# Kernel optimization log

Measured on AMD Instinct MI355X. Metric: run time of the kernel, lower is better.

## Reference

```python
import jax, jax.numpy as jnp
import numpy as np
from jax import lax

B, CIN, COUT, H, W, DG, K = 4, 128, 64, 128, 128, 16, 9
MAX_RES = 10.0  # max_residue_magnitude


def conv3x3(x, w, b):
    y = lax.conv_general_dilated(x, w, (1, 1), [(1, 1), (1, 1)],
                                 dimension_numbers=('NCHW', 'OIHW', 'NCHW'))
    return y + b[None, :, None, None]


def setup_inputs() -> dict:
    key = jax.random.key(0)
    ks = jax.random.split(key, 8)
    def rn(k, shape, s=0.05):
        return jax.random.normal(k, shape, jnp.float32) * s
    return {
        "x": jax.random.normal(ks[0], (B, CIN, H, W), jnp.float32),
        "extra_feat": jax.random.normal(ks[1], (B, 3 * COUT, H, W), jnp.float32),
        "w1": rn(ks[2], (COUT, 3 * COUT, 3, 3)), "b1": jnp.zeros((COUT,), jnp.float32),
        "w2": rn(ks[3], (COUT, COUT, 3, 3)), "b2": jnp.zeros((COUT,), jnp.float32),
        "w3": rn(ks[4], (COUT, COUT, 3, 3)), "b3": jnp.zeros((COUT,), jnp.float32),
        "w4": rn(ks[5], (27 * DG, COUT, 3, 3), 0.02), "b4": jnp.zeros((27 * DG,), jnp.float32),
        "weight": rn(ks[6], (COUT, CIN, 3, 3)), "bias": jnp.zeros((COUT,), jnp.float32),
    }


def deform_conv2d(x, offset, mask, weight, bias):
    # Modulated deformable conv, torchvision layout:
    # offset: [B, 2*DG*K, H, W] ordered (group, kernel_pos, (dy,dx))
    # mask:   [B, DG*K, H, W]
    Bn, Cin, Hh, Ww = x.shape
    Cg = Cin // DG
    off = offset.reshape(Bn, DG, K, 2, Hh, Ww)
    dy, dx = off[:, :, :, 0], off[:, :, :, 1]
    m = mask.reshape(Bn, DG, K, Hh, Ww)
    ki = (jnp.arange(K) // 3).reshape(1, 1, K, 1, 1).astype(x.dtype)
    kj = (jnp.arange(K) % 3).reshape(1, 1, K, 1, 1).astype(x.dtype)
    hh = jnp.arange(Hh, dtype=x.dtype).reshape(1, 1, 1, Hh, 1)
    ww = jnp.arange(Ww, dtype=x.dtype).reshape(1, 1, 1, 1, Ww)
    # sampling positions (stride=1, padding=1, dilation=1)
    py = hh - 1.0 + ki + dy  # [B,DG,K,H,W]
    px = ww - 1.0 + kj + dx
    y0 = jnp.floor(py)
    x0 = jnp.floor(px)
    ly = py - y0
    lx = px - x0
    xf = x.reshape(Bn, DG, Cg, Hh * Ww)

    def gather(yi, xi, wgt):
        valid = (yi >= 0) & (yi < Hh) & (xi >= 0) & (xi < Ww)
        yc = jnp.clip(yi, 0, Hh - 1).astype(jnp.int32)
        xc = jnp.clip(xi, 0, Ww - 1).astype(jnp.int32)
        idx = (yc * Ww + xc).reshape(Bn, DG, 1, K * Hh * Ww)
        g = jnp.take_along_axis(xf, jnp.broadcast_to(idx, (Bn, DG, Cg, K * Hh * Ww)), axis=3)
        g = g.reshape(Bn, DG, Cg, K, Hh, Ww)
        w_ = (wgt * valid.astype(x.dtype))[:, :, None]  # [B,DG,1,K,H,W]
        return g * w_

    val = (gather(y0, x0, (1 - ly) * (1 - lx))
           + gather(y0, x0 + 1, (1 - ly) * lx)
           + gather(y0 + 1, x0, ly * (1 - lx))
           + gather(y0 + 1, x0 + 1, ly * lx))
    val = val * m[:, :, None]  # modulation
    wk = weight.reshape(weight.shape[0], DG, Cg, K)
    out = jnp.einsum('bgckhw,ogck->bohw', val, wk) + bias[None, :, None, None]
    return out


def reference(x, extra_feat, w1, b1, w2, b2, w3, b3, w4, b4, weight, bias):
    lrelu = lambda t: jax.nn.leaky_relu(t, 0.1)
    t = lrelu(conv3x3(extra_feat, w1, b1))
    t = lrelu(conv3x3(t, w2, b2))
    t = lrelu(conv3x3(t, w3, b3))
    out = conv3x3(t, w4, b4)
    o1, o2, m = jnp.split(out, 3, axis=1)
    offset = MAX_RES * jnp.tanh(jnp.concatenate([o1, o2], axis=1))
    mask = jax.nn.sigmoid(m)
    return deform_conv2d(x, offset, mask, weight, bias)
```

## Files before the change

### kernel.cpp

```cpp
#include <hip/hip_runtime.h>
#include <cstdint>

#define H_ 128
#define W_ 128
#define HW 16384

typedef _Float16 f16x8 __attribute__((ext_vector_type(8)));
typedef _Float16 f16x4 __attribute__((ext_vector_type(4)));
typedef _Float16 f16x2 __attribute__((ext_vector_type(2)));
typedef float f32x4 __attribute__((ext_vector_type(4)));

__global__ __launch_bounds__(256)
void prep_all(const float* __restrict__ wd, const float* __restrict__ w1,
              const float* __restrict__ w2, const float* __restrict__ w3,
              const float* __restrict__ w4, const float* __restrict__ x,
              const float* __restrict__ ef,
              _Float16* __restrict__ wp, _Float16* __restrict__ A1,
              _Float16* __restrict__ A2, _Float16* __restrict__ A3,
              _Float16* __restrict__ A4, _Float16* __restrict__ xt,
              _Float16* __restrict__ ef_t) {
    __shared__ __align__(16) _Float16 t[128 * 200];
    const int bx  = blockIdx.x;
    const int tid = threadIdx.x;
    if (bx < 384) {
        int i = bx * 256 + tid;
        int kc = i % 96;
        int go = i / 96;
        int o = go & 63, g = go >> 6;
        float v = 0.f;
        if (kc < 72) { int k = kc >> 3, c = kc & 7; v = wd[(o * 128 + g * 8 + c) * 9 + k]; }
        wp[i] = (_Float16)v;
    } else if (bx < 2256) {
        const float* w; _Float16* Ap; int CIN, COUT, COpad, base;
        if (bx < 816)       { w = w1; Ap = A1; CIN = 192; COUT = 64;  COpad = 64;  base = 384; }
        else if (bx < 960)  { w = w2; Ap = A2; CIN = 64;  COUT = 64;  COpad = 64;  base = 816; }
        else if (bx < 1104) { w = w3; Ap = A3; CIN = 64;  COUT = 64;  COpad = 64;  base = 960; }
        else                { w = w4; Ap = A4; CIN = 64;  COUT = 432; COpad = 512; base = 1104; }
        int i = (bx - base) * 256 + tid;
        int kb = i / (COpad * 8);
        int rem = i - kb * (COpad * 8);
        int co = rem >> 3, j = rem & 7;
        int k = kb * 8 + j;
        int s = k / CIN;
        int ci = k - s * CIN;
        int kh = s / 3, kw = s % 3;
        float v = (co < COUT) ? w[((size_t)co * CIN + ci) * 9 + kh * 3 + kw] : 0.f;
        Ap[i] = (_Float16)v;
    } else if (bx < 6352) {
        int i = (bx - 2256) * 256 + tid;
        int px = i & 16383;
        int g  = (i >> 14) & 15;
        int b  = i >> 18;
        const float* xp = x + ((size_t)(b * 128 + g * 8) * HW) + px;
        f16x8 v;
        #pragma unroll
        for (int c = 0; c < 8; ++c) v[c] = (_Float16)xp[c * HW];
        *(f16x8*)(xt + (size_t)i * 8) = v;
    } else {
        int bb = bx - 6352;
        int b = bb >> 7, h = bb & 127;
        for (int i = tid; i < 192 * 128; i += 256) {
            int c = i >> 7, w = i & 127;
            t[w * 200 + c] = (_Float16)ef[((size_t)(b * 192 + c) * 128 + h) * 128 + w];
        }
        __syncthreads();
        _Float16* ob = ef_t + ((size_t)(b * 128 + h) * 128) * 192;
        for (int i = tid; i < 128 * 24; i += 256) {
            int px = i / 24, c8 = i % 24;
            *(f16x8*)(ob + px * 192 + c8 * 8) = *(const f16x8*)(t + px * 200 + c8 * 8);
        }
    }
}

template<int CIN_T, int COpad_T, int NWM, int NWN, int MT, int NT, int ACT>
__global__ __launch_bounds__(256)
void conv_mfma(const _Float16* __restrict__ in, const _Float16* __restrict__ Ap,
               const float* __restrict__ bias, void* __restrict__ outp,
               _Float16* __restrict__ mskp) {
    static_assert(NWM * NWN == 4 && NWN * NT * 16 == 128, "tiling");
    constexpr int NKH = (CIN_T == 64) ? 3 : 1;
    constexpr int NST = 3 / NKH;
    constexpr int CPC = CIN_T / 8;
    constexpr int TC  = NKH * 130 * CPC;
    __shared__ __align__(16) _Float16 lds[TC * 8];

    const int tid  = threadIdx.x;
    const int b    = blockIdx.x >> 7;
    const int h    = blockIdx.x & 127;
    const int cogB = blockIdx.y * (NWM * MT * 16);
    const int wv   = tid >> 6;
    const int wv_m = wv / NWN;
    const int wv_n = wv % NWN;
    const int lane = tid & 63;
    const int quad = lane >> 4;
    const int l16  = lane & 15;

    f32x4 acc[MT][NT];
    #pragma unroll
    for (int mt = 0; mt < MT; ++mt)
        #pragma unroll
        for (int nt = 0; nt < NT; ++nt) acc[mt][nt] = (f32x4){0.f, 0.f, 0.f, 0.f};

    const _Float16* inb = in + (size_t)b * (HW * CIN_T);

    #pragma unroll 1
    for (int s = 0; s < NST; ++s) {
        __syncthreads();
        for (int i = tid; i < TC; i += 256) {
            int kh_l = i / (130 * CPC);
            int r2   = i - kh_l * (130 * CPC);
            int wp_  = r2 / CPC;
            int c8   = r2 - wp_ * CPC;
            int kh   = s * NKH + kh_l;
            int hh   = h - 1 + kh;
            int w    = wp_ - 1;
            f16x8 v = (f16x8){0, 0, 0, 0, 0, 0, 0, 0};
            if ((unsigned)hh < 128u && (unsigned)w < 128u)
                v = *(const f16x8*)(inb + (hh * 128 + w) * CIN_T + c8 * 8);
            int slot = (c8 & ~7) | ((c8 & 7) ^ (wp_ & 7));
            ((f16x8*)lds)[(kh_l * 130 + wp_) * CPC + slot] = v;
        }
        __syncthreads();
        #pragma unroll
        for (int kh_l = 0; kh_l < NKH; ++kh_l) {
            const int kh = s * NKH + kh_l;
            #pragma unroll
            for (int kwi = 0; kwi < 3; ++kwi) {
                #pragma unroll
                for (int ci32 = 0; ci32 < CIN_T / 32; ++ci32) {
                    const int kb0 = (kh * 3 + kwi) * CPC + ci32 * 4;
                    f16x8 aF[MT];
                    #pragma unroll
                    for (int mt = 0; mt < MT; ++mt) {
                        int co_m = cogB + (wv_m * MT + mt) * 16 + l16;
                        aF[mt] = *(const f16x8*)(Ap + ((size_t)(kb0 + quad) * COpad_T + co_m) * 8);
                    }
                    const int c8v = ci32 * 4 + quad;
                    #pragma unroll
                    for (int nt = 0; nt < NT; ++nt) {
                        int n  = (wv_n * NT + nt) * 16 + l16;
                        int wq = n + kwi;
                        int slot = (c8v & ~7) | ((c8v & 7) ^ (wq & 7));
                        f16x8 bF = ((const f16x8*)lds)[(kh_l * 130 + wq) * CPC + slot];
                        #pragma unroll
                        for (int mt = 0; mt < MT; ++mt)
                            acc[mt][nt] = __builtin_amdgcn_mfma_f32_16x16x32_f16(aF[mt], bF, acc[mt][nt], 0, 0, 0);
                    }
                }
            }
        }
    }

    if (ACT == 1) {
        _Float16* ob = (_Float16*)outp + ((size_t)(b * 128 + h) * 128) * 64;
        #pragma unroll
        for (int mt = 0; mt < MT; ++mt) {
            int co_b = (wv_m * MT + mt) * 16 + quad * 4;
            #pragma unroll
            for (int nt = 0; nt < NT; ++nt) {
                int px = (wv_n * NT + nt) * 16 + l16;
                f16x4 sv;
                #pragma unroll
                for (int r = 0; r < 4; ++r) {
                    float v = acc[mt][nt][r] + bias[co_b + r];
                    v = v > 0.f ? v : 0.1f * v;
                    sv[r] = (_Float16)v;
                }
                *(f16x4*)(ob + px * 64 + co_b) = sv;
            }
        }
    } else {
        _Float16* off2 = (_Float16*)outp;
        #pragma unroll
        for (int mt = 0; mt < MT; ++mt) {
            int co_base = cogB + (wv_m * MT + mt) * 16 + quad * 4;
            #pragma unroll
            for (int r2 = 0; r2 < 2; ++r2) {
                int co0 = co_base + 2 * r2;
                if (co0 < 288) {
                    int g = co0 / 18;
                    int k = (co0 - g * 18) >> 1;
                    float bv0 = bias[co0], bv1 = bias[co0 + 1];
                    #pragma unroll
                    for (int nt = 0; nt < NT; ++nt) {
                        int px = (wv_n * NT + nt) * 16 + l16;
                        float v0 = acc[mt][nt][2 * r2]     + bv0;
                        float v1 = acc[mt][nt][2 * r2 + 1] + bv1;
                        float e0 = __expf(2.f * v0);
                        float e1 = __expf(2.f * v1);
                        f16x2 ov;
                        ov[0] = (_Float16)(10.f * (1.f - 2.f / (e0 + 1.f)));
                        ov[1] = (_Float16)(10.f * (1.f - 2.f / (e1 + 1.f)));
                        *(f16x2*)(off2 + (((size_t)(b * 16 + g) * 9 + k) * HW + h * 128 + px) * 2) = ov;
                    }
                } else if (co0 < 432) {
                    #pragma unroll
                    for (int j = 0; j < 2; ++j) {
                        int co = co0 + j;
                        int mm = co - 288;
                        int g = mm / 9;
                        int k = mm - g * 9;
                        float bv = bias[co];
                        #pragma unroll
                        for (int nt = 0; nt < NT; ++nt) {
                            int px = (wv_n * NT + nt) * 16 + l16;
                            float v = acc[mt][nt][2 * r2 + j] + bv;
                            v = 1.f / (1.f + __expf(-v));
                            mskp[((size_t)(b * 16 + g) * 9 + k) * HW + h * 128 + px] = (_Float16)v;
                        }
                    }
                }
            }
        }
    }
}

__global__ __launch_bounds__(256, 4)
void deform_fused(const _Float16* __restrict__ xt, const _Float16* __restrict__ off2,
                  const _Float16* __restrict__ msk, const _Float16* __restrict__ wp,
                  const float* __restrict__ bias, float* __restrict__ out) {
    __shared__ __align__(16) char vlds[2 * 64 * 256];
    const int tid  = threadIdx.x;
    const int bx   = (blockIdx.x & 7) * 128 + (blockIdx.x >> 3);
    const int ns   = bx & 1;
    const int bh   = bx >> 1;
    const int b    = bh >> 7;
    const int hrow = bh & 127;
    const int wv   = tid >> 6;
    const int lane = tid & 63;
    const int quad = lane >> 4;
    const int l16  = lane & 15;

    const int pxl   = tid & 63;
    const int kq    = tid >> 6;
    const int wglob = ns * 64 + pxl;
    const int pxg   = hrow * 128 + wglob;

    {
        f32x4 z = (f32x4){0.f, 0.f, 0.f, 0.f};
        for (int i = tid; i < 2048; i += 256) ((f32x4*)vlds)[i] = z;
    }
    __syncthreads();

    const _Float16* o2b = off2 + (size_t)b * 16 * 9 * HW * 2;
    const _Float16* mb  = msk  + (size_t)b * 16 * 9 * HW;

    f32x4 acc[4];
    #pragma unroll
    for (int nt = 0; nt < 4; ++nt) acc[nt] = (f32x4){0.f, 0.f, 0.f, 0.f};

    f16x2 od_c[3]; _Float16 m_c[3];
    #pragma unroll
    for (int i = 0; i < 3; ++i) {
        int k = kq + 4 * i;
        if (k < 9) {
            od_c[i] = *(const f16x2*)(o2b + ((size_t)(0 * 9 + k) * HW + pxg) * 2);
            m_c[i]  = mb[(size_t)(0 * 9 + k) * HW + pxg];
        }
    }

    #pragma unroll 1
    for (int gl = 0; gl < 16; ++gl) {
        const _Float16* xg = xt + ((size_t)(b * 16 + gl) * HW) * 8;
        char* vb = vlds + (gl & 1) * 16384;

        f16x8 aF[3];
        const _Float16* wg = wp + ((size_t)(gl * 64 + wv * 16 + l16)) * 96 + quad * 8;
        #pragma unroll
        for (int s = 0; s < 3; ++s) aF[s] = *(const f16x8*)(wg + s * 32);

        f16x2 od_n[3]; _Float16 m_n[3];
        if (gl < 15) {
            #pragma unroll
            for (int i = 0; i < 3; ++i) {
                int k = kq + 4 * i;
                if (k < 9) {
                    od_n[i] = *(const f16x2*)(o2b + ((size_t)((gl + 1) * 9 + k) * HW + pxg) * 2);
                    m_n[i]  = mb[(size_t)((gl + 1) * 9 + k) * HW + pxg];
                }
            }
        }

        #pragma unroll
        for (int i = 0; i < 3; ++i) {
            int k = kq + 4 * i;
            if (k < 9) {
                float dy = (float)od_c[i][0];
                float dx = (float)od_c[i][1];
                float m  = (float)m_c[i];
                float py  = (float)(hrow - 1 + k / 3) + dy;
                float pxf = (float)(wglob - 1 + k % 3) + dx;
                float y0f = floorf(py), x0f = floorf(pxf);
                float ly = py - y0f, lx = pxf - x0f;
                int y0 = (int)y0f, x0 = (int)x0f;
                int y1 = y0 + 1,  x1 = x0 + 1;
                float vy0 = ((unsigned)y0 < 128u) ? 1.f : 0.f;
                float vy1 = ((unsigned)y1 < 128u) ? 1.f : 0.f;
                float vx0 = ((unsigned)x0 < 128u) ? 1.f : 0.f;
                float vx1 = ((unsigned)x1 < 128u) ? 1.f : 0.f;
                float w00 = (1.f - ly) * (1.f - lx) * vy0 * vx0 * m;
                float w01 = (1.f - ly) * lx         * vy0 * vx1 * m;
                float w10 = ly * (1.f - lx)         * vy1 * vx0 * m;
                float w11 = ly * lx                 * vy1 * vx1 * m;
                int yc0 = min(max(y0, 0), 127), yc1 = min(max(y1, 0), 127);
                int xc0 = min(max(x0, 0), 127), xc1 = min(max(x1, 0), 127);
                f16x8 c00 = *(const f16x8*)(xg + (yc0 * W_ + xc0) * 8);
                f16x8 c01 = *(const f16x8*)(xg + (yc0 * W_ + xc1) * 8);
                f16x8 c10 = *(const f16x8*)(xg + (yc1 * W_ + xc0) * 8);
                f16x8 c11 = *(const f16x8*)(xg + (yc1 * W_ + xc1) * 8);
                _Float16 h00 = (_Float16)w00, h01 = (_Float16)w01;
                _Float16 h10 = (_Float16)w10, h11 = (_Float16)w11;
                f16x8 vv = c00 * h00 + c01 * h01 + c10 * h10 + c11 * h11;
                int chunk = k ^ (pxl & 15);
                *(f16x8*)(vb + pxl * 256 + chunk * 16) = vv;
            }
        }
        __syncthreads();

        #pragma unroll
        for (int nt = 0; nt < 4; ++nt) {
            int row = nt * 16 + l16;
            int sw  = row & 15;
            #pragma unroll
            for (int s = 0; s < 3; ++s) {
                f16x8 bF = *(const f16x8*)(vb + row * 256 + (((s << 2) + quad) ^ sw) * 16);
                acc[nt] = __builtin_amdgcn_mfma_f32_16x16x32_f16(aF[s], bF, acc[nt], 0, 0, 0);
            }
        }

        #pragma unroll
        for (int i = 0; i < 3; ++i) { od_c[i] = od_n[i]; m_c[i] = m_n[i]; }
    }

    __syncthreads();
    float* vf = (float*)vlds;
    #pragma unroll
    for (int r = 0; r < 4; ++r) {
        int o = wv * 16 + quad * 4 + r;
        #pragma unroll
        for (int nt = 0; nt < 4; ++nt) {
            int col = nt ^ quad;
            vf[o * 64 + col * 16 + l16] = acc[nt][r];
        }
    }
    __syncthreads();
    float* ob = out + ((size_t)(b * 64)) * HW + hrow * 128 + ns * 64;
    #pragma unroll
    for (int it = 0; it < 4; ++it) {
        int slot = tid + it * 256;
        int o    = slot >> 4;
        int p4   = slot & 15;
        int col  = (p4 >> 2) ^ ((o >> 2) & 3);
        f32x4 v = *(const f32x4*)(vf + o * 64 + col * 16 + (p4 & 3) * 4);
        float bv = bias[o];
        float4 sv = make_float4(v[0] + bv, v[1] + bv, v[2] + bv, v[3] + bv);
        *(float4*)(ob + (size_t)o * HW + p4 * 4) = sv;
    }
}

extern "C" void kernel_launch(void* const* d_in, const int* in_sizes, int n_in,
                              void* d_out, int out_size, void* d_ws, size_t ws_size,
                              hipStream_t stream) {
    const float* x  = (const float*)d_in[0];
    const float* ef = (const float*)d_in[1];
    const float* w1 = (const float*)d_in[2];
    const float* b1 = (const float*)d_in[3];
    const float* w2 = (const float*)d_in[4];
    const float* b2 = (const float*)d_in[5];
    const float* w3 = (const float*)d_in[6];
    const float* b3 = (const float*)d_in[7];
    const float* w4 = (const float*)d_in[8];
    const float* b4 = (const float*)d_in[9];
    const float* wd = (const float*)d_in[10];
    const float* bd = (const float*)d_in[11];
    float* out = (float*)d_out;

    char* ws = (char*)d_ws;
    _Float16* ef_t = (_Float16*)(ws);
    _Float16* tA   = (_Float16*)(ws + 25165824);
    _Float16* tB   = (_Float16*)(ws + 33554432);
    _Float16* off2 = (_Float16*)(ws + 41943040);
    _Float16* mskb = (_Float16*)(ws + 79691776);
    _Float16* wpd  = (_Float16*)(ws + 98566144);
    _Float16* A1   = (_Float16*)(ws + 98762752);
    _Float16* A2   = (_Float16*)(ws + 98983936);
    _Float16* A3   = (_Float16*)(ws + 99057664);
    _Float16* A4   = (_Float16*)(ws + 99131392);
    _Float16* xtb  = (_Float16*)(ws + 99721216);

    prep_all<<<6864, 256, 0, stream>>>(wd, w1, w2, w3, w4, x, ef,
                                       wpd, A1, A2, A3, A4, xtb, ef_t);

    conv_mfma<192, 64, 2, 2, 2, 4, 1><<<dim3(512, 1), 256, 0, stream>>>(ef_t, A1, b1, tA, nullptr);
    conv_mfma< 64, 64, 2, 2, 2, 4, 1><<<dim3(512, 1), 256, 0, stream>>>(tA, A2, b2, tB, nullptr);
    conv_mfma< 64, 64, 2, 2, 2, 4, 1><<<dim3(512, 1), 256, 0, stream>>>(tB, A3, b3, tA, nullptr);
    conv_mfma< 64, 512, 2, 2, 4, 4, 2><<<dim3(512, 4), 256, 0, stream>>>(tA, A4, b4, off2, mskb);

    deform_fused<<<1024, 256, 0, stream>>>(xtb, off2, mskb, wpd, bd, out);
}
```

Baseline: 348.4 us.

## Retile conv kernels to half-row tiles and loop output-channel groups in-block

```diff
diff --git a/kernel.cpp b/kernel.cpp
--- a/kernel.cpp
+++ b/kernel.cpp
@@ -72,28 +72,36 @@
     }
 }
 
-template<int CIN_T, int COpad_T, int NWM, int NWN, int MT, int NT, int ACT>
-__global__ __launch_bounds__(256)
-void conv_mfma(const _Float16* __restrict__ in, const _Float16* __restrict__ Ap,
-               const float* __restrict__ bias, void* __restrict__ outp,
-               _Float16* __restrict__ mskp) {
-    static_assert(NWM * NWN == 4 && NWN * NT * 16 == 128, "tiling");
+template<int CIN_T, int COUT_T, int COpad_T, int NWM, int NWN, int MT, int NT,
+         int ACT, int NGRP>
+__global__ __launch_bounds__(256, 4)
+void conv_mfma2(const _Float16* __restrict__ in, const _Float16* __restrict__ Ap,
+                const float* __restrict__ bias, void* __restrict__ outp,
+                _Float16* __restrict__ mskp) {
+    constexpr int PX = 64;
+    static_assert(NWM * NWN == 4 && NWN * NT * 16 == PX, "tiling");
+    constexpr int TW  = PX + 2;
+    constexpr int CPC = CIN_T / 8;
     constexpr int NKH = (CIN_T == 64) ? 3 : 1;
     constexpr int NST = 3 / NKH;
-    constexpr int CPC = CIN_T / 8;
-    constexpr int TC  = NKH * 130 * CPC;
+    static_assert(NGRP == 1 || NST == 1, "group loop needs single-stage LDS");
+    constexpr int TC  = NKH * TW * CPC;
+    constexpr int COg = NWM * MT * 16;
     __shared__ __align__(16) _Float16 lds[TC * 8];
 
     const int tid  = threadIdx.x;
-    const int b    = blockIdx.x >> 7;
-    const int h    = blockIdx.x & 127;
-    const int cogB = blockIdx.y * (NWM * MT * 16);
+    const int bxr  = (blockIdx.x & 7) * 128 + (blockIdx.x >> 3);
+    const int ns   = bxr & 1;
+    const int bh   = bxr >> 1;
+    const int b    = bh >> 7;
+    const int h    = bh & 127;
     const int wv   = tid >> 6;
     const int wv_m = wv / NWN;
-    const int wv_n = wv % NWN;
+    const int wv_n = wv - wv_m * NWN;
     const int lane = tid & 63;
     const int quad = lane >> 4;
     const int l16  = lane & 15;
+    const int w0g  = ns * PX;
 
     f32x4 acc[MT][NT];
     #pragma unroll
@@ -103,24 +111,24 @@
 
     const _Float16* inb = in + (size_t)b * (HW * CIN_T);
 
-    #pragma unroll 1
-    for (int s = 0; s < NST; ++s) {
-        __syncthreads();
+    auto stage = [&](int s) {
         for (int i = tid; i < TC; i += 256) {
-            int kh_l = i / (130 * CPC);
-            int r2   = i - kh_l * (130 * CPC);
+            int kh_l = i / (TW * CPC);
+            int r2   = i - kh_l * (TW * CPC);
             int wp_  = r2 / CPC;
             int c8   = r2 - wp_ * CPC;
             int kh   = s * NKH + kh_l;
             int hh   = h - 1 + kh;
-            int w    = wp_ - 1;
+            int w    = w0g + wp_ - 1;
             f16x8 v = (f16x8){0, 0, 0, 0, 0, 0, 0, 0};
             if ((unsigned)hh < 128u && (unsigned)w < 128u)
                 v = *(const f16x8*)(inb + (hh * 128 + w) * CIN_T + c8 * 8);
             int slot = (c8 & ~7) | ((c8 & 7) ^ (wp_ & 7));
-            ((f16x8*)lds)[(kh_l * 130 + wp_) * CPC + slot] = v;
-        }
-        __syncthreads();
+            ((f16x8*)lds)[(kh_l * TW + wp_) * CPC + slot] = v;
+        }
+    };
+
+    auto compute = [&](int s, int cogB, int mtmax) {
         #pragma unroll
         for (int kh_l = 0; kh_l < NKH; ++kh_l) {
             const int kh = s * NKH + kh_l;
@@ -131,7 +139,7 @@
                     const int kb0 = (kh * 3 + kwi) * CPC + ci32 * 4;
                     f16x8 aF[MT];
                     #pragma unroll
-                    for (int mt = 0; mt < MT; ++mt) {
+                    for (int mt = 0; mt < MT; ++mt) if (mt < mtmax) {
                         int co_m = cogB + (wv_m * MT + mt) * 16 + l16;
                         aF[mt] = *(const f16x8*)(Ap + ((size_t)(kb0 + quad) * COpad_T + co_m) * 8);
                     }
@@ -141,75 +149,109 @@
                         int n  = (wv_n * NT + nt) * 16 + l16;
                         int wq = n + kwi;
                         int slot = (c8v & ~7) | ((c8v & 7) ^ (wq & 7));
-                        f16x8 bF = ((const f16x8*)lds)[(kh_l * 130 + wq) * CPC + slot];
+                        f16x8 bF = ((const f16x8*)lds)[(kh_l * TW + wq) * CPC + slot];
                         #pragma unroll
-                        for (int mt = 0; mt < MT; ++mt)
+                        for (int mt = 0; mt < MT; ++mt) if (mt < mtmax)
                             acc[mt][nt] = __builtin_amdgcn_mfma_f32_16x16x32_f16(aF[mt], bF, acc[mt][nt], 0, 0, 0);
                     }
                 }
             }
         }
-    }
-
-    if (ACT == 1) {
-        _Float16* ob = (_Float16*)outp + ((size_t)(b * 128 + h) * 128) * 64;
-        #pragma unroll
-        for (int mt = 0; mt < MT; ++mt) {
-            int co_b = (wv_m * MT + mt) * 16 + quad * 4;
+    };
+
+    auto epilogue = [&](int cogB) {
+        if constexpr (ACT == 1) {
+            _Float16* ob = (_Float16*)outp + ((size_t)((b * 128 + h) * 128) + w0g) * 64;
             #pragma unroll
-            for (int nt = 0; nt < NT; ++nt) {
-                int px = (wv_n * NT + nt) * 16 + l16;
-                f16x4 sv;
+            for (int mt = 0; mt < MT; ++mt) {
+                int co_b = (wv_m * MT + mt) * 16 + quad * 4;
                 #pragma unroll
-                for (int r = 0; r < 4; ++r) {
-                    float v = acc[mt][nt][r] + bias[co_b + r];
-                    v = v > 0.f ? v : 0.1f * v;
-                    sv[r] = (_Float16)v;
+                for (int nt = 0; nt < NT; ++nt) {
+                    int px = (wv_n * NT + nt) * 16 + l16;
+                    f16x4 sv;
+                    #pragma unroll
+                    for (int r = 0; r < 4; ++r) {
+                        float v = acc[mt][nt][r] + bias[co_b + r];
+                        v = v > 0.f ? v : 0.1f * v;
+                        sv[r] = (_Float16)v;
+                    }
+                    *(f16x4*)(ob + px * 64 + co_b) = sv;
                 }
-                *(f16x4*)(ob + px * 64 + co_b) = sv;
-            }
-        }
-    } else {
-        _Float16* off2 = (_Float16*)outp;
-        #pragma unroll
-        for (int mt = 0; mt < MT; ++mt) {
-            int co_base = cogB + (wv_m * MT + mt) * 16 + quad * 4;
+            }
+        } else {
+            _Float16* off2 = (_Float16*)outp;
+            const int pxbase = h * 128 + w0g;
             #pragma unroll
-            for (int r2 = 0; r2 < 2; ++r2) {
-                int co0 = co_base + 2 * r2;
-                if (co0 < 288) {
-                    int g = co0 / 18;
-                    int k = (co0 - g * 18) >> 1;
-                    float bv0 = bias[co0], bv1 = bias[co0 + 1];
-                    #pragma unroll
-                    for (int nt = 0; nt < NT; ++nt) {
-                        int px = (wv_n * NT + nt) * 16 + l16;
-                        float v0 = acc[mt][nt][2 * r2]     + bv0;
-                        float v1 = acc[mt][nt][2 * r2 + 1] + bv1;
-                        float e0 = __expf(2.f * v0);
-                        float e1 = __expf(2.f * v1);
-                        f16x2 ov;
-                        ov[0] = (_Float16)(10.f * (1.f - 2.f / (e0 + 1.f)));
-                        ov[1] = (_Float16)(10.f * (1.f - 2.f / (e1 + 1.f)));
-                        *(f16x2*)(off2 + (((size_t)(b * 16 + g) * 9 + k) * HW + h * 128 + px) * 2) = ov;
-                    }
-                } else if (co0 < 432) {
-                    #pragma unroll
-                    for (int j = 0; j < 2; ++j) {
-                        int co = co0 + j;
-                        int mm = co - 288;
-                        int g = mm / 9;
-                        int k = mm - g * 9;
-                        float bv = bias[co];
+            for (int mt = 0; mt < MT; ++mt) {
+                int co_base = cogB + (wv_m * MT + mt) * 16 + quad * 4;
+                #pragma unroll
+                for (int r2 = 0; r2 < 2; ++r2) {
+                    int co0 = co_base + 2 * r2;
+                    if (co0 < 288) {
+                        int g = co0 / 18;
+                        int k = (co0 - g * 18) >> 1;
+                        float bv0 = bias[co0], bv1 = bias[co0 + 1];
                         #pragma unroll
                         for (int nt = 0; nt < NT; ++nt) {
                             int px = (wv_n * NT + nt) * 16 + l16;
-                            float v = acc[mt][nt][2 * r2 + j] + bv;
-                            v = 1.f / (1.f + __expf(-v));
-                            mskp[((size_t)(b * 16 + g) * 9 + k) * HW + h * 128 + px] = (_Float16)v;
+                            float v0 = acc[mt][nt][2 * r2]     + bv0;
+                            float v1 = acc[mt][nt][2 * r2 + 1] + bv1;
+                            float e0 = __expf(2.f * v0);
+                            float e1 = __expf(2.f * v1);
+                            f16x2 ov;
+                            ov[0] = (_Float16)(10.f * (1.f - 2.f / (e0 + 1.f)));
+                            ov[1] = (_Float16)(10.f * (1.f - 2.f / (e1 + 1.f)));
+                            *(f16x2*)(off2 + (((size_t)(b * 16 + g) * 9 + k) * HW + pxbase + px) * 2) = ov;
+                        }
+                    } else if (co0 < 432) {
+                        #pragma unroll
+                        for (int j = 0; j < 2; ++j) {
+                            int co = co0 + j;
+                            int mm = co - 288;
+                            int g = mm / 9;
+                            int k = mm - g * 9;
+                            float bv = bias[co];
+                            #pragma unroll
+                            for (int nt = 0; nt < NT; ++nt) {
+                                int px = (wv_n * NT + nt) * 16 + l16;
+                                float v = acc[mt][nt][2 * r2 + j] + bv;
+                                v = 1.f / (1.f + __expf(-v));
+                                mskp[((size_t)(b * 16 + g) * 9 + k) * HW + pxbase + px] = (_Float16)v;
+                            }
                         }
                     }
                 }
+            }
+        }
+    };
+
+    if constexpr (NGRP == 1) {
+        #pragma unroll 1
+        for (int s = 0; s < NST; ++s) {
+            __syncthreads();
+            stage(s);
+            __syncthreads();
+            compute(s, 0, MT);
+        }
+        epilogue(0);
+    } else {
+        stage(0);
+        __syncthreads();
+        #pragma unroll 1
+        for (int grp = 0; grp < NGRP; ++grp) {
+            const int cogB = grp * COg;
+            int rem = (COUT_T - cogB) / 16 - wv_m * MT;
+            int mtmax = rem < 0 ? 0 : (rem > MT ? MT : rem);
+            if (mtmax == MT)      compute(0, cogB, MT);
+            else if (mtmax == 3 && MT > 3) compute(0, cogB, 3);
+            else if (mtmax == 2 && MT > 2) compute(0, cogB, 2);
+            else if (mtmax == 1 && MT > 1) compute(0, cogB, 1);
+            epilogue(cogB);
+            if (grp + 1 < NGRP) {
+                #pragma unroll
+                for (int mt = 0; mt < MT; ++mt)
+                    #pragma unroll
+                    for (int nt = 0; nt < NT; ++nt) acc[mt][nt] = (f32x4){0.f, 0.f, 0.f, 0.f};
             }
         }
     }
@@ -391,10 +433,10 @@
     prep_all<<<6864, 256, 0, stream>>>(wd, w1, w2, w3, w4, x, ef,
                                        wpd, A1, A2, A3, A4, xtb, ef_t);
 
-    conv_mfma<192, 64, 2, 2, 2, 4, 1><<<dim3(512, 1), 256, 0, stream>>>(ef_t, A1, b1, tA, nullptr);
-    conv_mfma< 64, 64, 2, 2, 2, 4, 1><<<dim3(512, 1), 256, 0, stream>>>(tA, A2, b2, tB, nullptr);
-    conv_mfma< 64, 64, 2, 2, 2, 4, 1><<<dim3(512, 1), 256, 0, stream>>>(tB, A3, b3, tA, nullptr);
-    conv_mfma< 64, 512, 2, 2, 4, 4, 2><<<dim3(512, 4), 256, 0, stream>>>(tA, A4, b4, off2, mskb);
+    conv_mfma2<192,  64,  64,  2,  2, 2, 2, 1, 1><<<1024, 256, 0, stream>>>(ef_t, A1, b1, tA, nullptr);
+    conv_mfma2< 64,  64,  64,  2,  2, 2, 2, 1, 1><<<1024, 256, 0, stream>>>(tA, A2, b2, tB, nullptr);
+    conv_mfma2< 64,  64,  64,  2,  2, 2, 2, 1, 1><<<1024, 256, 0, stream>>>(tB, A3, b3, tA, nullptr);
+    conv_mfma2< 64, 432, 512,  4,  1, 4, 4, 2, 2><<<1024, 256, 0, stream>>>(tA, A4, b4, off2, mskb);
 
     deform_fused<<<1024, 256, 0, stream>>>(xtb, off2, mskb, wpd, bd, out);
 }
```

New measurement: 355.2 us. No clear change (+2.0%).
